# Kernel optimization log

Measured on AMD Instinct MI355X. Metric: run time of the kernel, lower is better.

The kernel has to match this reference:

```python
import jax, jax.numpy as jnp
from jax import lax
import numpy as np

DN = ('NCHW', 'OIHW', 'NCHW')
LEAKY_SLOPE = 0.01  # torch nn.LeakyReLU default


def conv(x, w, b=None, stride=1, pad=0):
    y = lax.conv_general_dilated(x, w, (stride, stride), [(pad, pad), (pad, pad)],
                                 dimension_numbers=DN)
    return y if b is None else y + b[None, :, None, None]


def conv_transpose2d(x, w, b):
    # torch ConvTranspose2d(k=4, s=2, p=1); w layout (Cin, Cout, 4, 4)
    wf = jnp.transpose(jnp.flip(w, (2, 3)), (1, 0, 2, 3))  # -> OIHW
    y = lax.conv_general_dilated(x, wf, (1, 1), [(2, 2), (2, 2)],
                                 lhs_dilation=(2, 2), dimension_numbers=DN)
    return y + b[None, :, None, None]


def residual_stack(x, rw3, rw1):
    # 6 ResidualLayers: x + conv1x1(relu(conv3x3(x))), both convs bias-free
    for i in range(rw3.shape[0]):
        h = jax.nn.relu(conv(x, rw3[i], pad=1))
        x = x + conv(h, rw1[i])
    return x


def vector_quantize(latents, codebook):
    # latents: [B, D, H, W] -> NHWC
    lat = jnp.transpose(latents, (0, 2, 3, 1))
    B, H, W, D = lat.shape
    flat = lat.reshape(-1, D)  # [N, D]
    # pairwise squared distances [N, K]
    dist = (jnp.sum(flat ** 2, axis=1, keepdims=True)
            + jnp.sum(codebook ** 2, axis=1)
            - 2.0 * flat @ codebook.T)
    inds = jnp.argmin(dist, axis=1)            # [N]
    q = codebook[inds].reshape(B, H, W, D)     # gather == one-hot matmul
    commitment_loss = jnp.mean((lax.stop_gradient(q) - lat) ** 2)
    embedding_loss = jnp.mean((q - lax.stop_gradient(lat)) ** 2)
    q_st = lat + lax.stop_gradient(q - lat)    # straight-through
    return jnp.transpose(q_st, (0, 3, 1, 2)), embedding_loss, commitment_loss


def setup_inputs() -> dict:
    key = jax.random.key(0)
    ks = iter(jax.random.split(key, 32))
    B, C, S = 16, 3, 128
    H0, H1 = 128, 256          # hidden_dims
    D, K = 64, 512             # embedding_dim, num_embeddings
    n_res = 6

    def w(shape, scale=0.05):
        return (jax.random.normal(next(ks), shape, dtype=jnp.float32) * scale)

    inp = {
        'x': jax.random.normal(next(ks), (B, C, S, S), dtype=jnp.float32),
        # encoder
        'ew0': w((H0, C, 4, 4)), 'eb0': jnp.zeros((H0,), jnp.float32),
        'ew1': w((H1, H0, 4, 4)), 'eb1': jnp.zeros((H1,), jnp.float32),
        'ew2': w((H1, H1, 3, 3)), 'eb2': jnp.zeros((H1,), jnp.float32),
        'erw3': w((n_res, H1, H1, 3, 3)),
        'erw1': w((n_res, H1, H1, 1, 1)),
        'ew3': w((D, H1, 1, 1)), 'eb3': jnp.zeros((D,), jnp.float32),
        # codebook, uniform(-1/K, 1/K) as in torch init
        'codebook': jax.random.uniform(next(ks), (K, D), jnp.float32, -1.0 / K, 1.0 / K),
        # decoder
        'dw0': w((H1, D, 3, 3)), 'db0': jnp.zeros((H1,), jnp.float32),
        'drw3': w((n_res, H1, H1, 3, 3)),
        'drw1': w((n_res, H1, H1, 1, 1)),
        'tw0': w((H1, H0, 4, 4)), 'tb0': jnp.zeros((H0,), jnp.float32),
        'tw1': w((H0, C, 4, 4)), 'tb1': jnp.zeros((C,), jnp.float32),
    }
    return inp


def reference(x, ew0, eb0, ew1, eb1, ew2, eb2, erw3, erw1, ew3, eb3,
              codebook, dw0, db0, drw3, drw1, tw0, tb0, tw1, tb1):
    lrelu = lambda t: jax.nn.leaky_relu(t, LEAKY_SLOPE)
    # encoder: two stride-2 downsamples, conv3x3, 6 residuals, 1x1 -> D
    h = lrelu(conv(x, ew0, eb0, stride=2, pad=1))   # [B,128,64,64]
    h = lrelu(conv(h, ew1, eb1, stride=2, pad=1))   # [B,256,32,32]
    h = lrelu(conv(h, ew2, eb2, stride=1, pad=1))
    h = residual_stack(h, erw3, erw1)
    h = lrelu(h)
    z = lrelu(conv(h, ew3, eb3))                    # [B,64,32,32]
    # vector quantization
    q, embedding_loss, commitment_loss = vector_quantize(z, codebook)
    # decoder
    d = lrelu(conv(q, dw0, db0, stride=1, pad=1))   # [B,256,32,32]
    d = residual_stack(d, drw3, drw1)
    d = lrelu(d)
    d = lrelu(conv_transpose2d(d, tw0, tb0))        # [B,128,64,64]
    recons = jnp.tanh(conv_transpose2d(d, tw1, tb1))  # [B,3,128,128]
    return recons, embedding_loss, commitment_loss
```

## Files before the change

kernel.cpp:

```cpp
#include <hip/hip_runtime.h>
#include <math.h>


typedef __attribute__((ext_vector_type(8))) short bf16x8;
typedef __attribute__((ext_vector_type(4))) float f32x4;

__device__ __forceinline__ float bf2f(short s) {
    unsigned u = ((unsigned)(unsigned short)s) << 16;
    return __builtin_bit_cast(float, u);
}
__device__ __forceinline__ unsigned short f2bfu(float f) {
    unsigned u = __builtin_bit_cast(unsigned, f);
    u = (u + 0x7fff + ((u >> 16) & 1)) >> 16;
    return (unsigned short)u;
}
__device__ __forceinline__ short f2bf(float f) { return (short)f2bfu(f); }
__device__ __forceinline__ int pack2(float a, float b) {
    return (int)f2bfu(a) | ((int)f2bfu(b) << 16);
}

template<int ACT>
__device__ __forceinline__ float actf(float v) {
    if (ACT == 1) return fmaxf(v, 0.f);
    if (ACT == 2) return v > 0.f ? v : 0.01f * v;
    return v;
}

__device__ __forceinline__ void gload_lds16(const void* g, void* l) {
    __builtin_amdgcn_global_load_lds(
        (const __attribute__((address_space(1))) unsigned int*)g,
        (__attribute__((address_space(3))) unsigned int*)l, 16, 0, 0);
}

__device__ __forceinline__ int fof(int r) { return (r & 3) ^ ((r >> 2) & 3); }

#define WAITV(N) asm volatile("s_waitcnt vmcnt(" #N ")" ::: "memory")
#define LGKM0 asm volatile("s_waitcnt lgkmcnt(0)" ::: "memory")

__device__ __forceinline__ void perm_one(const float* src, short* dst,
        int COUT, int CIN, int T, int i, int total) {
    if (i >= total) return;
    int ic = i % CIN; int r = i / CIN;
    int oc = r % COUT; r /= COUT;
    int t = r % T; int c = r / T;
    dst[i] = f2bf(src[(((size_t)c * COUT + oc) * CIN + ic) * T + t]);
}

__global__ __launch_bounds__(256) void prep_all_k(
        const float* ew1, const float* ew2, const float* erw3,
        const float* erw1, const float* ew3, const float* dw0,
        const float* drw3, const float* drw1, const float* tw0,
        short* Wp1, short* We2, short* Wer3, short* We11, short* Wz,
        short* Wd0, short* Wdr3, short* Wdr1, short* Wt0) {
    int bid = blockIdx.x, tid = threadIdx.x;
    if (bid < 2048) {
        perm_one(ew1, Wp1, 256, 128, 16, bid * 256 + tid, 524288);
    } else if (bid < 4352) {
        perm_one(ew2, We2, 256, 256, 9, (bid - 2048) * 256 + tid, 589824);
    } else if (bid < 18176) {
        perm_one(erw3, Wer3, 256, 256, 9, (bid - 4352) * 256 + tid, 3538944);
    } else if (bid < 19712) {
        perm_one(erw1, We11, 256, 256, 1, (bid - 18176) * 256 + tid, 393216);
    } else if (bid < 19776) {
        perm_one(ew3, Wz, 64, 256, 1, (bid - 19712) * 256 + tid, 16384);
    } else if (bid < 20352) {
        perm_one(dw0, Wd0, 256, 64, 9, (bid - 19776) * 256 + tid, 147456);
    } else if (bid < 34176) {
        perm_one(drw3, Wdr3, 256, 256, 9, (bid - 20352) * 256 + tid, 3538944);
    } else if (bid < 35712) {
        perm_one(drw1, Wdr1, 256, 256, 1, (bid - 34176) * 256 + tid, 393216);
    } else {
        int i = (bid - 35712) * 256 + tid;
        if (i < 524288) {
            int ic = i & 255; int r = i >> 8;
            int oc = r & 127; r >>= 7;
            int tap = r & 3; int par = r >> 2;
            int py = par >> 1, px = par & 1, my = tap >> 1, mx = tap & 1;
            int ky = 2 * my + (py ^ 1), kx = 2 * mx + (px ^ 1);
            Wt0[i] = f2bf(tw0[(((size_t)ic * 128 + oc) * 4 + ky) * 4 + kx]);
        }
    }
}

__global__ __launch_bounds__(256) void halo_all_k(short* P0, short* PB,
        short* PC, short* Pq) {
    int g = blockIdx.x * 256 + threadIdx.x;
    short* base; int W, C, idx;
    if (g < 135168)      { base = P0; W = 68; C = 128; idx = g; }
    else if (g < 274432) { base = PB; W = 36; C = 256; idx = g - 135168; }
    else if (g < 413696) { base = PC; W = 36; C = 256; idx = g - 274432; }
    else                 { base = Pq; W = 36; C = 64;  idx = g - 413696; }
    int c8 = C >> 3;
    int per_img = (4 * W + (W - 4) * 4) * c8;
    int img = idx / per_img, r = idx - img * per_img;
    int row, off;
    if (r < 4 * W * c8) {
        int rr = r / (W * c8);
        row = (rr < 2) ? rr : W - 4 + rr;
        off = r - rr * (W * c8);
    } else {
        int r2 = r - 4 * W * c8;
        row = 2 + r2 / (4 * c8);
        int q = r2 - (row - 2) * (4 * c8);
        off = (q < 2 * c8) ? q : (W - 2) * c8 + (q - 2 * c8);
    }
    ((int4*)(base + ((size_t)img * W + row) * W * C))[off] = int4{0, 0, 0, 0};
}

template<int CIN, int NTAPS, int TAPPAT, int SM, int INW, int OUTACT,
         bool HASB, bool FUSE>
__global__ __launch_bounds__(1024, 1) void rconv_k(
        const short* __restrict__ in, const short* __restrict__ Wp,
        const float* __restrict__ bias, const short* __restrict__ W1p,
        short* __restrict__ outp) {
    constexpr int CH64 = (CIN >= 128) ? CIN / 64 : 1;
    constexpr int LG2 = (CH64 == 4) ? 2 : (CH64 == 2) ? 1 : 0;
    constexpr int ST = NTAPS * CH64;
    __shared__ short sLds[81920];
    const int tid = threadIdx.x;
    const int lane = tid & 63, wv = tid >> 6;
    const int wc = wv & 3, mh = (wv >> 2) & 1, kg = wv >> 3;
    const int pix0 = blockIdx.x * 64;
    const int l15 = lane & 15, hi = lane >> 4;
    const int sl = hi ^ fof(l15);
    const bool low = (tid < 512);

    const short* Aptr = in;
    if (low) {
        int arow = tid >> 3, aslot = tid & 7;
        int pixa = pix0 + arow;
        int ba = pixa >> 10, Ya = (pixa >> 5) & 31, Xa = pixa & 31;
        Aptr = in + (size_t)((ba * INW + SM * Ya + 2) * INW + (SM * Xa + 2)) * CIN
             + (aslot >> 2) * 32 + (((aslot & 3) ^ fof(arow)) * 8);
    }
    const short* Bptr[2];
#pragma unroll
    for (int j = 0; j < 2; j++) {
        int gb = tid + 1024 * j;
        int kkb = gb >> 10, oc = (gb >> 2) & 255, slb = gb & 3;
        Bptr[j] = Wp + (size_t)oc * CIN + kkb * 32 + ((slb ^ fof(oc)) * 8);
    }

    auto stage = [&](int s, int bi) {
        int t = s >> LG2;
        int c0 = (s & (CH64 - 1)) * 64;
        int rof, cof;
        if (TAPPAT == 1) { rof = t / 3 - 1; cof = t % 3 - 1; }
        else             { rof = (t >> 2) - 1; cof = (t & 3) - 1; }
        char* L = (char*)sLds + bi * 40960;
        if (low)
            gload_lds16(Aptr + (rof * INW + cof) * CIN + c0, L + tid * 16);
        int woff = t * (256 * CIN) + c0;
        gload_lds16(Bptr[0] + woff, L + 8192 + tid * 16);
        gload_lds16(Bptr[1] + woff, L + 8192 + (tid + 1024) * 16);
    };

    f32x4 acc[2][4];
#pragma unroll
    for (int mi = 0; mi < 2; mi++)
#pragma unroll
        for (int ni = 0; ni < 4; ni++) acc[mi][ni] = f32x4{0.f, 0.f, 0.f, 0.f};

    stage(0, 0);
    stage(1, 1);
    int bi = 0;
    for (int s = 0; s < ST; ++s) {
        if (s < ST - 1) { if (low) { WAITV(3); } else { WAITV(2); } }
        else { WAITV(0); }
        __builtin_amdgcn_s_barrier();
        int nx = bi + 2; if (nx >= 3) nx -= 3;
        if (s + 2 < ST) stage(s + 2, nx);
        const short* LA = sLds + bi * 20480;
        const short* LB = LA + 4096;
        bf16x8 af[2], bfr[4];
#pragma unroll
        for (int mi = 0; mi < 2; mi++)
            af[mi] = *(const bf16x8*)(LA + (mh * 32 + mi * 16 + l15) * 64
                                      + kg * 32 + sl * 8);
#pragma unroll
        for (int ni = 0; ni < 4; ni++)
            bfr[ni] = *(const bf16x8*)(LB + kg * 8192
                                       + (wc * 64 + ni * 16 + l15) * 32 + sl * 8);
        __builtin_amdgcn_s_setprio(1);
#pragma unroll
        for (int mi = 0; mi < 2; mi++)
#pragma unroll
            for (int ni = 0; ni < 4; ni++)
                acc[mi][ni] = __builtin_amdgcn_mfma_f32_16x16x32_bf16(
                    af[mi], bfr[ni], acc[mi][ni], 0, 0, 0);
        __builtin_amdgcn_s_setprio(0);
        bi = (bi == 2) ? 0 : bi + 1;
    }

    float* MB = (float*)sLds;

    __syncthreads();
    if (kg == 1) {
#pragma unroll
        for (int mi = 0; mi < 2; mi++)
#pragma unroll
            for (int ni = 0; ni < 4; ni++)
#pragma unroll
                for (int r = 0; r < 4; r++)
                    MB[(mh * 32 + mi * 16 + hi * 4 + r) * 256
                       + wc * 64 + ni * 16 + l15] = acc[mi][ni][r];
    }
    __syncthreads();

    if (!FUSE) {
        if (kg == 0) {
#pragma unroll
            for (int mi = 0; mi < 2; mi++)
#pragma unroll
                for (int ni = 0; ni < 4; ni++) {
                    int col = wc * 64 + ni * 16 + l15;
                    float b = HASB ? bias[col] : 0.f;
#pragma unroll
                    for (int r = 0; r < 4; r++) {
                        int row = mh * 32 + mi * 16 + hi * 4 + r;
                        MB[row * 256 + col] += acc[mi][ni][r] + b;
                    }
                }
        }
        __syncthreads();
#pragma unroll
        for (int j = 0; j < 2; j++) {
            int idx = j * 1024 + tid;
            int p = idx >> 5, c0 = (idx & 31) * 8;
            int pix = pix0 + p;
            int b = pix >> 10, Y = (pix >> 5) & 31, X = pix & 31;
            size_t base = (((size_t)b * 36 + Y + 2) * 36 + X + 2) * 256 + c0;
            const float4* m4 = (const float4*)(MB + p * 256 + c0);
            float4 lo = m4[0], hv = m4[1];
            int pk[4];
            pk[0] = pack2(actf<OUTACT>(lo.x), actf<OUTACT>(lo.y));
            pk[1] = pack2(actf<OUTACT>(lo.z), actf<OUTACT>(lo.w));
            pk[2] = pack2(actf<OUTACT>(hv.x), actf<OUTACT>(hv.y));
            pk[3] = pack2(actf<OUTACT>(hv.z), actf<OUTACT>(hv.w));
            *(int4*)(outp + base) = *(int4*)pk;
        }
        return;
    }

    const short* W1ptr[2];
#pragma unroll
    for (int j = 0; j < 2; j++) {
        int gb = tid + 1024 * j;
        int kkb = gb >> 10, oc = (gb >> 2) & 255, slb = gb & 3;
        W1ptr[j] = W1p + (size_t)oc * 256 + kkb * 32 + ((slb ^ fof(oc)) * 8);
    }
    auto stage2 = [&](int c) {
        char* L = (char*)sLds + 98304 + (c & 1) * 32768;
        gload_lds16(W1ptr[0] + c * 64, L + tid * 16);
        gload_lds16(W1ptr[1] + c * 64, L + (tid + 1024) * 16);
    };
    stage2(0);
    stage2(1);

    short* H = sLds + 32768;
    if (kg == 0) {
#pragma unroll
        for (int mi = 0; mi < 2; mi++)
#pragma unroll
            for (int ni = 0; ni < 4; ni++) {
                int col = wc * 64 + ni * 16 + l15;
#pragma unroll
                for (int r = 0; r < 4; r++) {
                    int row = mh * 32 + mi * 16 + hi * 4 + r;
                    float v = acc[mi][ni][r] + MB[row * 256 + col];
                    H[((col >> 5) * 64 + row) * 32
                      + (((col >> 3) & 3) ^ fof(row)) * 8 + (col & 7)]
                        = f2bf(fmaxf(v, 0.f));
                }
            }
    }
    LGKM0;
    __builtin_amdgcn_sched_barrier(0);
    __builtin_amdgcn_s_barrier();

    f32x4 acc2[2][4];
#pragma unroll
    for (int mi = 0; mi < 2; mi++)
#pragma unroll
        for (int ni = 0; ni < 4; ni++) acc2[mi][ni] = f32x4{0.f, 0.f, 0.f, 0.f};

    for (int s2 = 0; s2 < 4; ++s2) {
        if (s2 < 3) { WAITV(2); } else { WAITV(0); }
        __builtin_amdgcn_s_barrier();
        int c = s2 * 2 + kg;
        const short* LW = sLds + 49152 + (s2 & 1) * 16384 + kg * 8192;
        bf16x8 af2[2], bf2r[4];
#pragma unroll
        for (int mi = 0; mi < 2; mi++) {
            int row = mh * 32 + mi * 16 + l15;
            af2[mi] = *(const bf16x8*)(H + (c * 64 + row) * 32
                                       + (hi ^ fof(row)) * 8);
        }
#pragma unroll
        for (int ni = 0; ni < 4; ni++)
            bf2r[ni] = *(const bf16x8*)(LW + (wc * 64 + ni * 16 + l15) * 32
                                        + sl * 8);
        LGKM0;
        __builtin_amdgcn_sched_barrier(0);
        __builtin_amdgcn_s_barrier();
        if (s2 < 2) stage2(s2 + 2);
        __builtin_amdgcn_s_setprio(1);
#pragma unroll
        for (int mi = 0; mi < 2; mi++)
#pragma unroll
            for (int ni = 0; ni < 4; ni++)
                acc2[mi][ni] = __builtin_amdgcn_mfma_f32_16x16x32_bf16(
                    af2[mi], bf2r[ni], acc2[mi][ni], 0, 0, 0);
        __builtin_amdgcn_s_setprio(0);
    }

    __syncthreads();
    if (kg == 1) {
#pragma unroll
        for (int mi = 0; mi < 2; mi++)
#pragma unroll
            for (int ni = 0; ni < 4; ni++)
#pragma unroll
                for (int r = 0; r < 4; r++)
                    MB[(mh * 32 + mi * 16 + hi * 4 + r) * 256
                       + wc * 64 + ni * 16 + l15] = acc2[mi][ni][r];
    }
    __syncthreads();
    if (kg == 0) {
#pragma unroll
        for (int mi = 0; mi < 2; mi++)
#pragma unroll
            for (int ni = 0; ni < 4; ni++) {
                int col = wc * 64 + ni * 16 + l15;
#pragma unroll
                for (int r = 0; r < 4; r++) {
                    int row = mh * 32 + mi * 16 + hi * 4 + r;
                    MB[row * 256 + col] += acc2[mi][ni][r];
                }
            }
    }
    __syncthreads();
#pragma unroll
    for (int j = 0; j < 2; j++) {
        int idx = j * 1024 + tid;
        int p = idx >> 5, c0 = (idx & 31) * 8;
        int pix = pix0 + p;
        int b = pix >> 10, Y = (pix >> 5) & 31, X = pix & 31;
        size_t base = (((size_t)b * 36 + Y + 2) * 36 + X + 2) * 256 + c0;
        const float4* m4 = (const float4*)(MB + p * 256 + c0);
        float4 lo = m4[0], hv = m4[1];
        bf16x8 rv = *(const bf16x8*)(in + base);
        int pk[4];
        pk[0] = pack2(actf<OUTACT>(lo.x + bf2f(rv[0])),
                      actf<OUTACT>(lo.y + bf2f(rv[1])));
        pk[1] = pack2(actf<OUTACT>(lo.z + bf2f(rv[2])),
                      actf<OUTACT>(lo.w + bf2f(rv[3])));
        pk[2] = pack2(actf<OUTACT>(hv.x + bf2f(rv[4])),
                      actf<OUTACT>(hv.y + bf2f(rv[5])));
        pk[3] = pack2(actf<OUTACT>(hv.z + bf2f(rv[6])),
                      actf<OUTACT>(hv.w + bf2f(rv[7])));
        *(int4*)(outp + base) = *(int4*)pk;
    }
}

template<int CIN, int COUT, int NTAPS, int TAPPAT, int SM, int INW,
         int OUTACT, bool RES, bool HASB, int OUTMODE, int BN>
__global__ __launch_bounds__(256) void gconv_k(
        const short* __restrict__ in, const short* __restrict__ Wp,
        const float* __restrict__ bias, const short* __restrict__ res,
        void* __restrict__ outp) {
    constexpr int KCH = CIN / 32;
    constexpr int LG = (KCH == 8) ? 3 : (KCH == 4) ? 2 : (KCH == 2) ? 1 : 0;
    constexpr int ST = NTAPS * KCH;
    constexpr int NF = BN / 32;
    constexpr int WN = BN / 2;
    __shared__ short sA[3 * 128 * 32];
    __shared__ short sB[3 * BN * 32];
    const int tid = threadIdx.x;
    const int lane = tid & 63, wv = tid >> 6;
    const int wr = wv >> 1, wc = wv & 1;
    const int pix0 = blockIdx.x * 128;
    const int oc0 = blockIdx.y * BN;
    int py = 0, px = 0;
    if (TAPPAT == 3) {
        int par = blockIdx.z;
        py = par >> 1; px = par & 1;
        Wp += (size_t)par * NTAPS * COUT * CIN;
    }
    const int sp = tid >> 2;
    const int swz = ((tid & 3) ^ fof(sp)) * 8;
    int rbA[2];
#pragma unroll
    for (int rd = 0; rd < 2; rd++) {
        int pix = pix0 + sp + rd * 64;
        int b = pix >> 10, Y = (pix >> 5) & 31, X = pix & 31;
        rbA[rd] = ((b * INW + SM * Y + 2) * INW + (SM * X + 2)) * CIN + swz;
    }
    const int wb0 = (oc0 + sp) * CIN + swz;
    const int wb1 = (oc0 + sp + 64) * CIN + swz;

    f32x4 acc[4][NF];
#pragma unroll
    for (int i = 0; i < 4; i++)
#pragma unroll
        for (int j = 0; j < NF; j++) acc[i][j] = f32x4{0.f, 0.f, 0.f, 0.f};

    const int sslot = ((lane >> 4) ^ fof(lane & 15)) * 8;
    const int abase = (wr * 64 + (lane & 15)) * 32 + sslot;
    const int bbase = (wc * WN + (lane & 15)) * 32 + sslot;

    auto stage = [&](int s, int biq) {
        int t = s >> LG, c = s & (KCH - 1);
        int rof, cof;
        if (TAPPAT == 0) { rof = 0; cof = 0; }
        else if (TAPPAT == 1) { rof = t / 3 - 1; cof = t % 3 - 1; }
        else if (TAPPAT == 2) { rof = t / 4 - 1; cof = t % 4 - 1; }
        else { int my = t >> 1, mx = t & 1;
               rof = (py == 0) ? -my : 1 - my;
               cof = (px == 0) ? -mx : 1 - mx; }
        const int tapoff = (rof * INW + cof) * CIN + c * 32;
        char* a = (char*)sA + biq * 8192;
        char* b = (char*)sB + biq * (BN * 64);
        const short* wt = Wp + (size_t)t * COUT * CIN + c * 32;
        gload_lds16(in + rbA[0] + tapoff, a + tid * 16);
        gload_lds16(in + rbA[1] + tapoff, a + 4096 + tid * 16);
        gload_lds16(wt + wb0, b + tid * 16);
        if (BN == 128) gload_lds16(wt + wb1, b + 4096 + tid * 16);
    };

    stage(0, 0);
    stage(1, 1);
    int cur = 0;
    for (int s = 0; s < ST; ++s) {
        if (s < ST - 1) {
            if (BN == 128) { WAITV(4); } else { WAITV(3); }
        } else {
            WAITV(0);
        }
        __builtin_amdgcn_s_barrier();
        int nxt = cur + 2; if (nxt >= 3) nxt -= 3;
        if (s + 2 < ST) stage(s + 2, nxt);
        const short* a = sA + cur * 4096;
        const short* b = sB + cur * (BN * 32);
        bf16x8 af[4], bfm[NF];
#pragma unroll
        for (int mi = 0; mi < 4; mi++)
            af[mi] = *(const bf16x8*)(a + abase + mi * 512);
#pragma unroll
        for (int ni = 0; ni < NF; ni++)
            bfm[ni] = *(const bf16x8*)(b + bbase + ni * 512);
        __builtin_amdgcn_s_setprio(1);
#pragma unroll
        for (int mi = 0; mi < 4; mi++)
#pragma unroll
            for (int ni = 0; ni < NF; ni++)
                acc[mi][ni] = __builtin_amdgcn_mfma_f32_16x16x32_bf16(
                    af[mi], bfm[ni], acc[mi][ni], 0, 0, 0);
        __builtin_amdgcn_s_setprio(0);
        cur = (cur == 2) ? 0 : cur + 1;
    }
#pragma unroll
    for (int mi = 0; mi < 4; mi++) {
#pragma unroll
        for (int r = 0; r < 4; r++) {
            int pix = pix0 + wr * 64 + mi * 16 + (lane >> 4) * 4 + r;
            int b = pix >> 10, Y = (pix >> 5) & 31, X = pix & 31;
            size_t rowoff = 0;
            if (OUTMODE == 0)
                rowoff = (((size_t)b * 36 + Y + 2) * 36 + X + 2) * COUT;
            else if (OUTMODE == 2)
                rowoff = (((size_t)b * 68 + 2 * Y + py + 2) * 68 + 2 * X + px + 2) * 128;
#pragma unroll
            for (int ni = 0; ni < NF; ni++) {
                int col = oc0 + wc * WN + ni * 16 + (lane & 15);
                float v = acc[mi][ni][r];
                if (HASB) v += bias[col];
                if (OUTMODE == 1) {
                    ((float*)outp)[(size_t)pix * COUT + col] = actf<OUTACT>(v);
                } else {
                    size_t off = rowoff + col;
                    if (RES) v += bf2f(res[off]);
                    ((short*)outp)[off] = f2bf(actf<OUTACT>(v));
                }
            }
        }
    }
}

__global__ __launch_bounds__(256) void conv0_k(const float* __restrict__ x,
        const float* __restrict__ W, const float* __restrict__ bias,
        short* __restrict__ P0) {
    __shared__ float sP[3 * 4 * 132];
    __shared__ short sB[8192];
    __shared__ float sMB[8192];
    int y = blockIdx.x, b = blockIdx.y;
    int tid = threadIdx.x;
    int lane = tid & 63, w = tid >> 6;
    int l15 = lane & 15, hi = lane >> 4;
    int sl = hi ^ fof(l15);
    for (int t = tid; t < 8192; t += 256) {
        int oc = t >> 6, k = t & 63;
        float v = (k < 48) ? W[(size_t)oc * 48 + k] : 0.f;
        int kk = k >> 5, slot = (k >> 3) & 3, j = k & 7;
        sB[oc * 64 + kk * 32 + ((slot ^ fof(oc)) * 8) + j] = f2bf(v);
    }
    for (int t = tid; t < 1560; t += 256) {
        int ic = t / 520; int r = t - ic * 520;
        int ry = r / 130, rx = r - ry * 130;
        int iy = 2 * y - 1 + ry, ix = rx - 1;
        float v = 0.f;
        if ((unsigned)iy < 128u && (unsigned)ix < 128u)
            v = x[((size_t)b * 3 + ic) * 16384 + iy * 128 + ix];
        sP[(ic * 4 + ry) * 132 + rx] = v;
    }
    __syncthreads();
    int ox = w * 16 + l15;
    bf16x8 af[2];
#pragma unroll
    for (int kk = 0; kk < 2; kk++) {
        short tmp[8];
#pragma unroll
        for (int j = 0; j < 8; j++) {
            int k = kk * 32 + hi * 8 + j;
            float v = 0.f;
            if (k < 48) {
                int ic = k >> 4, ky = (k >> 2) & 3, kx = k & 3;
                v = sP[(ic * 4 + ky) * 132 + 2 * ox + kx];
            }
            tmp[j] = f2bf(v);
        }
        af[kk] = *(bf16x8*)tmp;
    }
    f32x4 acc[8];
#pragma unroll
    for (int ni = 0; ni < 8; ni++) acc[ni] = f32x4{0.f, 0.f, 0.f, 0.f};
#pragma unroll
    for (int ni = 0; ni < 8; ni++) {
        int oc = ni * 16 + l15;
        bf16x8 b0 = *(const bf16x8*)(sB + oc * 64 + sl * 8);
        bf16x8 b1 = *(const bf16x8*)(sB + oc * 64 + 32 + sl * 8);
        acc[ni] = __builtin_amdgcn_mfma_f32_16x16x32_bf16(af[0], b0, acc[ni], 0, 0, 0);
        acc[ni] = __builtin_amdgcn_mfma_f32_16x16x32_bf16(af[1], b1, acc[ni], 0, 0, 0);
    }
#pragma unroll
    for (int ni = 0; ni < 8; ni++) {
        int col = ni * 16 + l15;
        float bv = bias[col];
#pragma unroll
        for (int r = 0; r < 4; r++)
            sMB[(w * 16 + hi * 4 + r) * 128 + col] = actf<2>(acc[ni][r] + bv);
    }
    __syncthreads();
#pragma unroll
    for (int it = 0; it < 4; it++) {
        int idx = it * 256 + tid;
        int p = idx >> 4, c0 = (idx & 15) * 8;
        size_t base = (((size_t)b * 68 + y + 2) * 68 + p + 2) * 128 + c0;
        const float4* m4 = (const float4*)(sMB + p * 128 + c0);
        float4 lo = m4[0], hv = m4[1];
        int pk[4];
        pk[0] = pack2(lo.x, lo.y); pk[1] = pack2(lo.z, lo.w);
        pk[2] = pack2(hv.x, hv.y); pk[3] = pack2(hv.z, hv.w);
        *(int4*)(P0 + base) = *(int4*)pk;
    }
}

__global__ __launch_bounds__(256) void vq_argmin_k(const float* __restrict__ zr,
        const float* __restrict__ cb, int* __restrict__ ind) {
    __shared__ short sZ[2][128 * 32];
    __shared__ short sC[2][128 * 32];
    __shared__ float sN[128];
    const int tid = threadIdx.x;
    const int lane = tid & 63, wv = tid >> 6;
    const int pos0 = blockIdx.x * 128;
#pragma unroll
    for (int it = 0; it < 4; ++it) {
        int task = tid + it * 256;
        int row = task >> 3, kq = task & 7;
        const float4* zp = (const float4*)(zr + (size_t)(pos0 + row) * 64 + kq * 8);
        float4 v0 = zp[0], v1 = zp[1];
        int slot = ((kq & 3) ^ fof(row)) * 8;
        short tmp[8] = {f2bf(v0.x), f2bf(v0.y), f2bf(v0.z), f2bf(v0.w),
                        f2bf(v1.x), f2bf(v1.y), f2bf(v1.z), f2bf(v1.w)};
        *(bf16x8*)&sZ[kq >> 2][row * 32 + slot] = *(bf16x8*)tmp;
    }
    const int sslot = ((lane >> 4) ^ fof(lane & 15)) * 8;
    const int l15 = lane & 15;
    float best[2][4]; int bidx[2][4];
#pragma unroll
    for (int mi = 0; mi < 2; mi++)
#pragma unroll
        for (int r = 0; r < 4; r++) { best[mi][r] = INFINITY; bidx[mi][r] = 0; }
    for (int ch = 0; ch < 4; ++ch) {
        __syncthreads();
#pragma unroll
        for (int it = 0; it < 4; ++it) {
            int task = tid + it * 256;
            int row = task >> 3, kq = task & 7;
            const float4* cp = (const float4*)(cb + (size_t)(ch * 128 + row) * 64 + kq * 8);
            float4 v0 = cp[0], v1 = cp[1];
            int slot = ((kq & 3) ^ fof(row)) * 8;
            short tmp[8] = {f2bf(v0.x), f2bf(v0.y), f2bf(v0.z), f2bf(v0.w),
                            f2bf(v1.x), f2bf(v1.y), f2bf(v1.z), f2bf(v1.w)};
            *(bf16x8*)&sC[kq >> 2][row * 32 + slot] = *(bf16x8*)tmp;
        }
        if (tid < 128) {
            const float4* cp = (const float4*)(cb + (size_t)(ch * 128 + tid) * 64);
            float s = 0.f;
#pragma unroll
            for (int q = 0; q < 16; q++) {
                float4 v = cp[q];
                s += v.x * v.x + v.y * v.y + v.z * v.z + v.w * v.w;
            }
            sN[tid] = s;
        }
        __syncthreads();
        f32x4 acc[2][8];
#pragma unroll
        for (int mi = 0; mi < 2; mi++)
#pragma unroll
            for (int ni = 0; ni < 8; ni++) acc[mi][ni] = f32x4{0.f, 0.f, 0.f, 0.f};
#pragma unroll
        for (int kc = 0; kc < 2; ++kc) {
            bf16x8 za[2], ca[8];
#pragma unroll
            for (int mi = 0; mi < 2; mi++)
                za[mi] = *(const bf16x8*)&sZ[kc][(wv * 32 + mi * 16 + l15) * 32 + sslot];
#pragma unroll
            for (int ni = 0; ni < 8; ni++)
                ca[ni] = *(const bf16x8*)&sC[kc][(ni * 16 + l15) * 32 + sslot];
#pragma unroll
            for (int mi = 0; mi < 2; mi++)
#pragma unroll
                for (int ni = 0; ni < 8; ni++)
                    acc[mi][ni] = __builtin_amdgcn_mfma_f32_16x16x32_bf16(
                        za[mi], ca[ni], acc[mi][ni], 0, 0, 0);
        }
#pragma unroll
        for (int mi = 0; mi < 2; mi++)
#pragma unroll
            for (int ni = 0; ni < 8; ni++) {
                float nrm = sN[ni * 16 + l15];
                int idx = ch * 128 + ni * 16 + l15;
#pragma unroll
                for (int r = 0; r < 4; r++) {
                    float sc = nrm - 2.f * acc[mi][ni][r];
                    if (sc < best[mi][r]) { best[mi][r] = sc; bidx[mi][r] = idx; }
                }
            }
    }
#pragma unroll
    for (int m = 1; m < 16; m <<= 1) {
#pragma unroll
        for (int mi = 0; mi < 2; mi++)
#pragma unroll
            for (int r = 0; r < 4; r++) {
                float os = __shfl_xor(best[mi][r], m);
                int   oi = __shfl_xor(bidx[mi][r], m);
                if (os < best[mi][r] || (os == best[mi][r] && oi < bidx[mi][r])) {
                    best[mi][r] = os; bidx[mi][r] = oi;
                }
            }
    }
    if (l15 == 0) {
        int g = lane >> 4;
#pragma unroll
        for (int mi = 0; mi < 2; mi++)
#pragma unroll
            for (int r = 0; r < 4; r++)
                ind[pos0 + wv * 32 + mi * 16 + g * 4 + r] = bidx[mi][r];
    }
}

__global__ __launch_bounds__(256) void vq_gather_k(const float* __restrict__ zr,
        const float* __restrict__ cb, const int* __restrict__ ind,
        short* __restrict__ q, float* __restrict__ part) {
    int pos = blockIdx.x * 256 + threadIdx.x;
    int b = pos >> 10, hw = pos & 1023, y = hw >> 5, xx = hw & 31;
    int idx = ind[pos];
    const float4* cp = (const float4*)(cb + (size_t)idx * 64);
    const float4* zp = (const float4*)(zr + (size_t)pos * 64);
    size_t qb = (((size_t)b * 36 + y + 2) * 36 + xx + 2) * 64;
    float sum = 0.f;
#pragma unroll
    for (int d4 = 0; d4 < 16; d4++) {
        float4 c = cp[d4], z = zp[d4];
        float dx = c.x - z.x, dy = c.y - z.y, dz = c.z - z.z, dw = c.w - z.w;
        sum += dx * dx + dy * dy + dz * dz + dw * dw;
        ((int*)(q + qb))[2 * d4] = pack2(c.x, c.y);
        ((int*)(q + qb))[2 * d4 + 1] = pack2(c.z, c.w);
    }
#pragma unroll
    for (int m = 1; m < 64; m <<= 1) sum += __shfl_xor(sum, m);
    __shared__ float sred[4];
    int lane = threadIdx.x & 63, wvv = threadIdx.x >> 6;
    if (lane == 0) sred[wvv] = sum;
    __syncthreads();
    if (threadIdx.x == 0)
        part[blockIdx.x] = sred[0] + sred[1] + sred[2] + sred[3];
}

__global__ void finalize_k(const float* __restrict__ part, float* __restrict__ out) {
    if (threadIdx.x == 0) {
        float s = 0.f;
        for (int k = 0; k < 64; k++) s += part[k];
        float m = s / 1048576.f;
        out[786432] = m;
        out[786433] = m;
    }
}

__global__ __launch_bounds__(256) void tw1_k(const short* __restrict__ in,
        const float* __restrict__ W, const float* __restrict__ bias,
        float* __restrict__ out) {
    __shared__ float sW[16 * 128 * 4];
    int b = blockIdx.y, y0 = blockIdx.x * 8;
    int tid = threadIdx.x;
    for (int t = tid; t < 2048; t += 256) {
        int k = t >> 7, ic = t & 127;
        float4 v;
        v.x = W[((size_t)ic * 3 + 0) * 16 + k];
        v.y = W[((size_t)ic * 3 + 1) * 16 + k];
        v.z = W[((size_t)ic * 3 + 2) * 16 + k];
        v.w = 0.f;
        *(float4*)&sW[t * 4] = v;
    }
    __syncthreads();
    int r = tid >> 5, g = tid & 31;
    int oy = y0 + r, py = oy & 1, Y = oy >> 1, pxp = g & 1;
    float acc[4][3];
#pragma unroll
    for (int p = 0; p < 4; p++)
#pragma unroll
        for (int o = 0; o < 3; o++) acc[p][o] = 0.f;
#pragma unroll
    for (int my = 0; my < 2; my++) {
        int iy = Y + ((py == 0) ? -my : 1 - my) + 2;
        const short* rowp = in + (((size_t)b * 68 + iy) * 68) * 128;
        int ky = 2 * my + (py ^ 1);
#pragma unroll
        for (int mx = 0; mx < 2; mx++) {
            int kx = 2 * mx + (pxp ^ 1);
            int cof = ((pxp == 0) ? -mx : 1 - mx) + 2;
            const float* wbase = &sW[((ky * 4 + kx) * 128) * 4];
            const short* pptr[4];
#pragma unroll
            for (int p = 0; p < 4; p++) {
                int X = ((g + 32 * p) >> 1) + cof;
                pptr[p] = rowp + (size_t)X * 128;
            }
            for (int icb = 0; icb < 16; icb++) {
                bf16x8 v[4];
#pragma unroll
                for (int p = 0; p < 4; p++)
                    v[p] = *(const bf16x8*)(pptr[p] + icb * 8);
#pragma unroll
                for (int j = 0; j < 8; j++) {
                    float4 w = *(const float4*)&wbase[(icb * 8 + j) * 4];
#pragma unroll
                    for (int p = 0; p < 4; p++) {
                        float xv = bf2f(v[p][j]);
                        acc[p][0] += w.x * xv;
                        acc[p][1] += w.y * xv;
                        acc[p][2] += w.z * xv;
                    }
                }
            }
        }
    }
#pragma unroll
    for (int p = 0; p < 4; p++) {
        int ox = g + 32 * p;
#pragma unroll
        for (int o = 0; o < 3; o++)
            out[(((size_t)b * 3 + o) << 14) + oy * 128 + ox] =
                tanhf(acc[p][o] + bias[o]);
    }
}

extern "C" void kernel_launch(void* const* d_in, const int* in_sizes, int n_in,
                              void* d_out, int out_size, void* d_ws, size_t ws_size,
                              hipStream_t stream) {
    const float* x    = (const float*)d_in[0];
    const float* ew0  = (const float*)d_in[1];
    const float* eb0  = (const float*)d_in[2];
    const float* ew1  = (const float*)d_in[3];
    const float* eb1  = (const float*)d_in[4];
    const float* ew2  = (const float*)d_in[5];
    const float* eb2  = (const float*)d_in[6];
    const float* erw3 = (const float*)d_in[7];
    const float* erw1 = (const float*)d_in[8];
    const float* ew3  = (const float*)d_in[9];
    const float* eb3  = (const float*)d_in[10];
    const float* cbk  = (const float*)d_in[11];
    const float* dw0  = (const float*)d_in[12];
    const float* db0  = (const float*)d_in[13];
    const float* drw3 = (const float*)d_in[14];
    const float* drw1 = (const float*)d_in[15];
    const float* tw0  = (const float*)d_in[16];
    const float* tb0  = (const float*)d_in[17];
    const float* tw1  = (const float*)d_in[18];
    const float* tb1  = (const float*)d_in[19];
    float* out = (float*)d_out;

    short* S = (short*)d_ws;
    short* P0  = S;
    short* PB  = P0 + 9469952;
    short* PC  = PB + 5308416;
    short* Pq  = PC + 5308416;
    short* Wp1 = Pq + 1327104;
    short* We2 = Wp1 + 524288;
    short* Wer3 = We2 + 589824;
    short* We11 = Wer3 + 3538944;
    short* Wz   = We11 + 393216;
    short* Wd0  = Wz + 16384;
    short* Wdr3 = Wd0 + 147456;
    short* Wdr1 = Wdr3 + 3538944;
    short* Wt0  = Wdr1 + 393216;
    float* F   = (float*)(S + 31080448);
    float* Zr  = F;
    float* PART = Zr + 1048576;
    int*   IND = (int*)(PART + 64);

    halo_all_k<<<1752, 256, 0, stream>>>(P0, PB, PC, Pq);
    prep_all_k<<<37760, 256, 0, stream>>>(ew1, ew2, erw3, erw1, ew3, dw0,
        drw3, drw1, tw0, Wp1, We2, Wer3, We11, Wz, Wd0, Wdr3, Wdr1, Wt0);

    conv0_k<<<dim3(64, 16), 256, 0, stream>>>(x, ew0, eb0, P0);
    rconv_k<128, 16, 2, 2, 68, 2, true, false>
        <<<256, 1024, 0, stream>>>(P0, Wp1, eb1, nullptr, PB);
    rconv_k<256, 9, 1, 1, 36, 2, true, false>
        <<<256, 1024, 0, stream>>>(PB, We2, eb2, nullptr, PC);
    for (int i = 0; i < 6; i++) {
        short* inb  = (i & 1) ? PB : PC;
        short* outb = (i & 1) ? PC : PB;
        if (i < 5)
            rconv_k<256, 9, 1, 1, 36, 0, false, true>
                <<<256, 1024, 0, stream>>>(inb, Wer3 + (size_t)i * 589824,
                    nullptr, We11 + (size_t)i * 65536, outb);
        else
            rconv_k<256, 9, 1, 1, 36, 2, false, true>
                <<<256, 1024, 0, stream>>>(inb, Wer3 + (size_t)i * 589824,
                    nullptr, We11 + (size_t)i * 65536, outb);
    }
    gconv_k<256, 64, 1, 0, 1, 36, 2, false, true, 1, 64>
        <<<dim3(128, 1), 256, 0, stream>>>(PC, Wz, eb3, nullptr, Zr);

    vq_argmin_k<<<128, 256, 0, stream>>>(Zr, cbk, IND);
    vq_gather_k<<<64, 256, 0, stream>>>(Zr, cbk, IND, Pq, PART);

    rconv_k<64, 9, 1, 1, 36, 2, true, false>
        <<<256, 1024, 0, stream>>>(Pq, Wd0, db0, nullptr, PC);
    for (int i = 0; i < 6; i++) {
        short* inb  = (i & 1) ? PB : PC;
        short* outb = (i & 1) ? PC : PB;
        if (i < 5)
            rconv_k<256, 9, 1, 1, 36, 0, false, true>
                <<<256, 1024, 0, stream>>>(inb, Wdr3 + (size_t)i * 589824,
                    nullptr, Wdr1 + (size_t)i * 65536, outb);
        else
            rconv_k<256, 9, 1, 1, 36, 2, false, true>
                <<<256, 1024, 0, stream>>>(inb, Wdr3 + (size_t)i * 589824,
                    nullptr, Wdr1 + (size_t)i * 65536, outb);
    }
    gconv_k<256, 128, 4, 3, 1, 36, 2, false, true, 2, 128>
        <<<dim3(128, 1, 4), 256, 0, stream>>>(PC, Wt0, tb0, nullptr, P0);
    tw1_k<<<dim3(16, 16), 256, 0, stream>>>(P0, tw1, tb1, out);

    finalize_k<<<1, 64, 0, stream>>>(PART, out);
}
```

Baseline: 595.1 us.

## Halve rconv block to 512 threads and load weights directly into registers

The residual conv kernel now runs with 8 waves instead of 16, and each wave computes a 64x64 tile (4x4 MFMA fragments) instead of 32x64. Weight (B) fragments are no longer staged through LDS. Each lane loads them from global memory straight into double-buffered registers two steps ahead, while the activation tile still goes through a 3-stage LDS ring with a new XOR swizzle. The aim is to cut LDS traffic and barrier cost per MFMA and to raise arithmetic intensity per wave. The costs are higher register pressure, fewer waves to hide latency, and uncoalesced direct global weight loads.

Result: slower. 861.6 us (+44.8%).

```diff
diff --git a/kernel.cpp b/kernel.cpp
--- a/kernel.cpp
+++ b/kernel.cpp
@@ -109,7 +109,7 @@
 
 template<int CIN, int NTAPS, int TAPPAT, int SM, int INW, int OUTACT,
          bool HASB, bool FUSE>
-__global__ __launch_bounds__(1024, 1) void rconv_k(
+__global__ __launch_bounds__(512, 1) void rconv_k(
         const short* __restrict__ in, const short* __restrict__ Wp,
         const float* __restrict__ bias, const short* __restrict__ W1p,
         short* __restrict__ outp) {
@@ -119,113 +119,132 @@
     __shared__ short sLds[81920];
     const int tid = threadIdx.x;
     const int lane = tid & 63, wv = tid >> 6;
-    const int wc = wv & 3, mh = (wv >> 2) & 1, kg = wv >> 3;
+    const int wc = wv & 3, kg = wv >> 2;
     const int pix0 = blockIdx.x * 64;
     const int l15 = lane & 15, hi = lane >> 4;
-    const int sl = hi ^ fof(l15);
-    const bool low = (tid < 512);
-
-    const short* Aptr = in;
-    if (low) {
-        int arow = tid >> 3, aslot = tid & 7;
+
+    const int arow = tid >> 3, aslot = tid & 7;
+    const short* Aptr;
+    {
         int pixa = pix0 + arow;
         int ba = pixa >> 10, Ya = (pixa >> 5) & 31, Xa = pixa & 31;
+        int sk = (((aslot >> 2) ^ (arow >> 2)) & 1) * 32
+               + (((aslot & 3) ^ arow) & 3) * 8;
         Aptr = in + (size_t)((ba * INW + SM * Ya + 2) * INW + (SM * Xa + 2)) * CIN
-             + (aslot >> 2) * 32 + (((aslot & 3) ^ fof(arow)) * 8);
-    }
-    const short* Bptr[2];
-#pragma unroll
-    for (int j = 0; j < 2; j++) {
-        int gb = tid + 1024 * j;
-        int kkb = gb >> 10, oc = (gb >> 2) & 255, slb = gb & 3;
-        Bptr[j] = Wp + (size_t)oc * CIN + kkb * 32 + ((slb ^ fof(oc)) * 8);
-    }
-
-    auto stage = [&](int s, int bi) {
+             + sk;
+    }
+    auto stageA = [&](int s, int bi) {
         int t = s >> LG2;
         int c0 = (s & (CH64 - 1)) * 64;
         int rof, cof;
         if (TAPPAT == 1) { rof = t / 3 - 1; cof = t % 3 - 1; }
         else             { rof = (t >> 2) - 1; cof = (t & 3) - 1; }
-        char* L = (char*)sLds + bi * 40960;
-        if (low)
-            gload_lds16(Aptr + (rof * INW + cof) * CIN + c0, L + tid * 16);
-        int woff = t * (256 * CIN) + c0;
-        gload_lds16(Bptr[0] + woff, L + 8192 + tid * 16);
-        gload_lds16(Bptr[1] + woff, L + 8192 + (tid + 1024) * 16);
+        gload_lds16(Aptr + (rof * INW + cof) * CIN + c0,
+                    (char*)sLds + bi * 8192 + tid * 16);
     };
 
-    f32x4 acc[2][4];
-#pragma unroll
-    for (int mi = 0; mi < 2; mi++)
+    const short* Bb = Wp + (size_t)(wc * 64 + l15) * CIN + kg * 32 + hi * 8;
+    auto loadB = [&](int s, bf16x8 (&B)[4]) {
+        int t = s >> LG2;
+        int c0 = (s & (CH64 - 1)) * 64;
+        size_t off = (size_t)t * 256 * CIN + c0;
+#pragma unroll
+        for (int ni = 0; ni < 4; ni++)
+            B[ni] = *(const bf16x8*)(Bb + off + (size_t)ni * 16 * CIN);
+    };
+
+    f32x4 acc[4][4];
+#pragma unroll
+    for (int mi = 0; mi < 4; mi++)
 #pragma unroll
         for (int ni = 0; ni < 4; ni++) acc[mi][ni] = f32x4{0.f, 0.f, 0.f, 0.f};
 
-    stage(0, 0);
-    stage(1, 1);
-    int bi = 0;
-    for (int s = 0; s < ST; ++s) {
-        if (s < ST - 1) { if (low) { WAITV(3); } else { WAITV(2); } }
-        else { WAITV(0); }
+    auto body = [&](int s, int bi, bf16x8 (&Bc)[4]) {
+        if (s < ST - 1) { WAITV(5); } else { WAITV(0); }
         __builtin_amdgcn_s_barrier();
-        int nx = bi + 2; if (nx >= 3) nx -= 3;
-        if (s + 2 < ST) stage(s + 2, nx);
-        const short* LA = sLds + bi * 20480;
-        const short* LB = LA + 4096;
-        bf16x8 af[2], bfr[4];
-#pragma unroll
-        for (int mi = 0; mi < 2; mi++)
-            af[mi] = *(const bf16x8*)(LA + (mh * 32 + mi * 16 + l15) * 64
-                                      + kg * 32 + sl * 8);
-#pragma unroll
-        for (int ni = 0; ni < 4; ni++)
-            bfr[ni] = *(const bf16x8*)(LB + kg * 8192
-                                       + (wc * 64 + ni * 16 + l15) * 32 + sl * 8);
+        int nb = bi + 2; if (nb >= 3) nb -= 3;
+        if (s + 2 < ST) stageA(s + 2, nb);
+        const char* LA = (const char*)sLds + bi * 8192;
+        bf16x8 af[4];
+#pragma unroll
+        for (int mi = 0; mi < 4; mi++) {
+            int row = mi * 16 + l15;
+            af[mi] = *(const bf16x8*)(LA + row * 128
+                     + ((kg ^ (row >> 2)) & 1) * 64 + ((hi ^ row) & 3) * 16);
+        }
         __builtin_amdgcn_s_setprio(1);
 #pragma unroll
-        for (int mi = 0; mi < 2; mi++)
+        for (int mi = 0; mi < 4; mi++)
 #pragma unroll
             for (int ni = 0; ni < 4; ni++)
                 acc[mi][ni] = __builtin_amdgcn_mfma_f32_16x16x32_bf16(
-                    af[mi], bfr[ni], acc[mi][ni], 0, 0, 0);
+                    af[mi], Bc[ni], acc[mi][ni], 0, 0, 0);
         __builtin_amdgcn_s_setprio(0);
+        if (s + 2 < ST) loadB(s + 2, Bc);
+    };
+
+    bf16x8 B0[4], B1[4];
+    stageA(0, 0); loadB(0, B0);
+    stageA(1, 1); loadB(1, B1);
+    int bi = 0;
+#pragma unroll 2
+    for (int s = 0; s < ST; ++s) {
+        if (s & 1) body(s, bi, B1); else body(s, bi, B0);
         bi = (bi == 2) ? 0 : bi + 1;
     }
 
     float* MB = (float*)sLds;
+    short* H  = sLds + 32768;
+
+    const short* W1ptr[4];
+    if (FUSE) {
+#pragma unroll
+        for (int j = 0; j < 4; j++) {
+            int gb = tid + 512 * j;
+            int kkb = gb >> 10, oc = (gb >> 2) & 255, slb = gb & 3;
+            W1ptr[j] = W1p + (size_t)oc * 256 + kkb * 32 + ((slb ^ fof(oc)) * 8);
+        }
+    }
+    auto stage2 = [&](int c) {
+        char* L = (char*)sLds + 98304 + (c & 1) * 32768;
+#pragma unroll
+        for (int j = 0; j < 4; j++)
+            gload_lds16(W1ptr[j] + c * 64, L + (tid + 512 * j) * 16);
+    };
 
     __syncthreads();
+    if (FUSE) { stage2(0); stage2(1); }
     if (kg == 1) {
 #pragma unroll
-        for (int mi = 0; mi < 2; mi++)
+        for (int mi = 0; mi < 4; mi++)
 #pragma unroll
             for (int ni = 0; ni < 4; ni++)
 #pragma unroll
                 for (int r = 0; r < 4; r++)
-                    MB[(mh * 32 + mi * 16 + hi * 4 + r) * 256
-                       + wc * 64 + ni * 16 + l15] = acc[mi][ni][r];
+                    MB[(mi * 16 + hi * 4 + r) * 256 + wc * 64 + ni * 16 + l15]
+                        = acc[mi][ni][r];
     }
     __syncthreads();
 
     if (!FUSE) {
         if (kg == 0) {
 #pragma unroll
-            for (int mi = 0; mi < 2; mi++)
+            for (int mi = 0; mi < 4; mi++)
 #pragma unroll
                 for (int ni = 0; ni < 4; ni++) {
                     int col = wc * 64 + ni * 16 + l15;
                     float b = HASB ? bias[col] : 0.f;
 #pragma unroll
                     for (int r = 0; r < 4; r++) {
-                        int row = mh * 32 + mi * 16 + hi * 4 + r;
+                        int row = mi * 16 + hi * 4 + r;
                         MB[row * 256 + col] += acc[mi][ni][r] + b;
                     }
                 }
         }
         __syncthreads();
 #pragma unroll
-        for (int j = 0; j < 2; j++) {
-            int idx = j * 1024 + tid;
+        for (int j = 0; j < 4; j++) {
+            int idx = j * 512 + tid;
             int p = idx >> 5, c0 = (idx & 31) * 8;
             int pix = pix0 + p;
             int b = pix >> 10, Y = (pix >> 5) & 31, X = pix & 31;
@@ -242,31 +261,15 @@
         return;
     }
 
-    const short* W1ptr[2];
-#pragma unroll
-    for (int j = 0; j < 2; j++) {
-        int gb = tid + 1024 * j;
-        int kkb = gb >> 10, oc = (gb >> 2) & 255, slb = gb & 3;
-        W1ptr[j] = W1p + (size_t)oc * 256 + kkb * 32 + ((slb ^ fof(oc)) * 8);
-    }
-    auto stage2 = [&](int c) {
-        char* L = (char*)sLds + 98304 + (c & 1) * 32768;
-        gload_lds16(W1ptr[0] + c * 64, L + tid * 16);
-        gload_lds16(W1ptr[1] + c * 64, L + (tid + 1024) * 16);
-    };
-    stage2(0);
-    stage2(1);
-
-    short* H = sLds + 32768;
     if (kg == 0) {
 #pragma unroll
-        for (int mi = 0; mi < 2; mi++)
+        for (int mi = 0; mi < 4; mi++)
 #pragma unroll
             for (int ni = 0; ni < 4; ni++) {
                 int col = wc * 64 + ni * 16 + l15;
 #pragma unroll
                 for (int r = 0; r < 4; r++) {
-                    int row = mh * 32 + mi * 16 + hi * 4 + r;
+                    int row = mi * 16 + hi * 4 + r;
                     float v = acc[mi][ni][r] + MB[row * 256 + col];
                     H[((col >> 5) * 64 + row) * 32
                       + (((col >> 3) & 3) ^ fof(row)) * 8 + (col & 7)]
@@ -278,35 +281,36 @@
     __builtin_amdgcn_sched_barrier(0);
     __builtin_amdgcn_s_barrier();
 
-    f32x4 acc2[2][4];
-#pragma unroll
-    for (int mi = 0; mi < 2; mi++)
+    f32x4 acc2[4][4];
+#pragma unroll
+    for (int mi = 0; mi < 4; mi++)
 #pragma unroll
         for (int ni = 0; ni < 4; ni++) acc2[mi][ni] = f32x4{0.f, 0.f, 0.f, 0.f};
 
     for (int s2 = 0; s2 < 4; ++s2) {
-        if (s2 < 3) { WAITV(2); } else { WAITV(0); }
+        if (s2 < 3) { WAITV(4); } else { WAITV(0); }
         __builtin_amdgcn_s_barrier();
         int c = s2 * 2 + kg;
         const short* LW = sLds + 49152 + (s2 & 1) * 16384 + kg * 8192;
-        bf16x8 af2[2], bf2r[4];
-#pragma unroll
-        for (int mi = 0; mi < 2; mi++) {
-            int row = mh * 32 + mi * 16 + l15;
+        bf16x8 af2[4], bf2r[4];
+#pragma unroll
+        for (int mi = 0; mi < 4; mi++) {
+            int row = mi * 16 + l15;
             af2[mi] = *(const bf16x8*)(H + (c * 64 + row) * 32
-                                       + (hi ^ fof(row)) * 8);
-        }
-#pragma unroll
-        for (int ni = 0; ni < 4; ni++)
-            bf2r[ni] = *(const bf16x8*)(LW + (wc * 64 + ni * 16 + l15) * 32
-                                        + sl * 8);
+                                       + ((hi ^ fof(row)) & 3) * 8);
+        }
+#pragma unroll
+        for (int ni = 0; ni < 4; ni++) {
+            int row = wc * 64 + ni * 16 + l15;
+            bf2r[ni] = *(const bf16x8*)(LW + row * 32 + ((hi ^ fof(row)) & 3) * 8);
+        }
         LGKM0;
         __builtin_amdgcn_sched_barrier(0);
         __builtin_amdgcn_s_barrier();
         if (s2 < 2) stage2(s2 + 2);
         __builtin_amdgcn_s_setprio(1);
 #pragma unroll
-        for (int mi = 0; mi < 2; mi++)
+        for (int mi = 0; mi < 4; mi++)
 #pragma unroll
             for (int ni = 0; ni < 4; ni++)
                 acc2[mi][ni] = __builtin_amdgcn_mfma_f32_16x16x32_bf16(
@@ -317,32 +321,32 @@
     __syncthreads();
     if (kg == 1) {
 #pragma unroll
-        for (int mi = 0; mi < 2; mi++)
+        for (int mi = 0; mi < 4; mi++)
 #pragma unroll
             for (int ni = 0; ni < 4; ni++)
 #pragma unroll
                 for (int r = 0; r < 4; r++)
-                    MB[(mh * 32 + mi * 16 + hi * 4 + r) * 256
-                       + wc * 64 + ni * 16 + l15] = acc2[mi][ni][r];
+                    MB[(mi * 16 + hi * 4 + r) * 256 + wc * 64 + ni * 16 + l15]
+                        = acc2[mi][ni][r];
     }
     __syncthreads();
     if (kg == 0) {
 #pragma unroll
-        for (int mi = 0; mi < 2; mi++)
+        for (int mi = 0; mi < 4; mi++)
 #pragma unroll
             for (int ni = 0; ni < 4; ni++) {
                 int col = wc * 64 + ni * 16 + l15;
 #pragma unroll
                 for (int r = 0; r < 4; r++) {
-                    int row = mh * 32 + mi * 16 + hi * 4 + r;
+                    int row = mi * 16 + hi * 4 + r;
                     MB[row * 256 + col] += acc2[mi][ni][r];
                 }
             }
     }
     __syncthreads();
 #pragma unroll
-    for (int j = 0; j < 2; j++) {
-        int idx = j * 1024 + tid;
+    for (int j = 0; j < 4; j++) {
+        int idx = j * 512 + tid;
         int p = idx >> 5, c0 = (idx & 31) * 8;
         int pix = pix0 + p;
         int b = pix >> 10, Y = (pix >> 5) & 31, X = pix & 31;
@@ -828,19 +832,19 @@
 
     conv0_k<<<dim3(64, 16), 256, 0, stream>>>(x, ew0, eb0, P0);
     rconv_k<128, 16, 2, 2, 68, 2, true, false>
-        <<<256, 1024, 0, stream>>>(P0, Wp1, eb1, nullptr, PB);
+        <<<256, 512, 0, stream>>>(P0, Wp1, eb1, nullptr, PB);
     rconv_k<256, 9, 1, 1, 36, 2, true, false>
-        <<<256, 1024, 0, stream>>>(PB, We2, eb2, nullptr, PC);
+        <<<256, 512, 0, stream>>>(PB, We2, eb2, nullptr, PC);
     for (int i = 0; i < 6; i++) {
         short* inb  = (i & 1) ? PB : PC;
         short* outb = (i & 1) ? PC : PB;
         if (i < 5)
             rconv_k<256, 9, 1, 1, 36, 0, false, true>
-                <<<256, 1024, 0, stream>>>(inb, Wer3 + (size_t)i * 589824,
+                <<<256, 512, 0, stream>>>(inb, Wer3 + (size_t)i * 589824,
                     nullptr, We11 + (size_t)i * 65536, outb);
         else
             rconv_k<256, 9, 1, 1, 36, 2, false, true>
-                <<<256, 1024, 0, stream>>>(inb, Wer3 + (size_t)i * 589824,
+                <<<256, 512, 0, stream>>>(inb, Wer3 + (size_t)i * 589824,
                     nullptr, We11 + (size_t)i * 65536, outb);
     }
     gconv_k<256, 64, 1, 0, 1, 36, 2, false, true, 1, 64>
@@ -850,17 +854,17 @@
     vq_gather_k<<<64, 256, 0, stream>>>(Zr, cbk, IND, Pq, PART);
 
     rconv_k<64, 9, 1, 1, 36, 2, true, false>
-        <<<256, 1024, 0, stream>>>(Pq, Wd0, db0, nullptr, PC);
+        <<<256, 512, 0, stream>>>(Pq, Wd0, db0, nullptr, PC);
     for (int i = 0; i < 6; i++) {
         short* inb  = (i & 1) ? PB : PC;
         short* outb = (i & 1) ? PC : PB;
         if (i < 5)
             rconv_k<256, 9, 1, 1, 36, 0, false, true>
-                <<<256, 1024, 0, stream>>>(inb, Wdr3 + (size_t)i * 589824,
+                <<<256, 512, 0, stream>>>(inb, Wdr3 + (size_t)i * 589824,
                     nullptr, Wdr1 + (size_t)i * 65536, outb);
         else
             rconv_k<256, 9, 1, 1, 36, 2, false, true>
-                <<<256, 1024, 0, stream>>>(inb, Wdr3 + (size_t)i * 589824,
+                <<<256, 512, 0, stream>>>(inb, Wdr3 + (size_t)i * 589824,
                     nullptr, Wdr1 + (size_t)i * 65536, outb);
     }
     gconv_k<256, 128, 4, 3, 1, 36, 2, false, true, 2, 128>
```
